# Performance work log

Hardware: AMD Instinct MI355X
Metric: run time of the kernel (lower is better)

## Reference

```python
import jax, jax.numpy as jnp
from jax import lax
import numpy as np

B, C, L, HOP = 16, 64, 16384, 256
KS = 3        # LVC / conv kernel size
DIL = 3       # static Conv1d dilation (init arg)
KL = L // HOP # kernel_length (number of conditioning frames)


def setup_inputs() -> dict:
    key = jax.random.key(0)
    k0, k1, k2, k3 = jax.random.split(key, 4)
    return {
        "hidden_states": jax.random.normal(k0, (B, C, L), jnp.float32),
        "kernel": jax.random.normal(k1, (B, C, 2 * C, KS, KL), jnp.float32) * 0.05,
        "bias": jax.random.normal(k2, (B, 2 * C, KL), jnp.float32) * 0.05,
        "conv_w": jax.random.normal(k3, (C, C, KS), jnp.float32) * 0.05,
        "conv_b": jnp.zeros((C,), jnp.float32),
        "hop_size": HOP,
    }


def _lvc(x, kernel, bias, hop_size):
    # location-variable convolution; forward() uses dilation=1 here
    b, c, length = x.shape
    _, _, out_ch, ksize, klen = kernel.shape
    pad = (ksize - 1) // 2
    xp = jnp.pad(x, ((0, 0), (0, 0), (pad, pad)))
    # sliding windows of size ksize, stride 1 -> (b, c, length, ksize)
    win = jnp.stack([xp[:, :, i:i + length] for i in range(ksize)], axis=-1)
    # split time into (kernel_length, hop_size) frames
    win = win.reshape(b, c, klen, hop_size, ksize)
    # per-frame conv kernel contraction
    o = jnp.einsum('bilsk,biokl->bols', win, kernel)  # (b, out_ch, klen, hop)
    o = o + bias[:, :, :, None]
    return o.reshape(b, out_ch, klen * hop_size)


def reference(hidden_states, kernel, bias, conv_w, conv_b, hop_size):
    slope = 0.2
    pad = DIL * (KS - 1) // 2
    residual = hidden_states
    h = jax.nn.leaky_relu(hidden_states, slope)
    h = lax.conv_general_dilated(
        h, conv_w, window_strides=(1,), padding=[(pad, pad)],
        rhs_dilation=(DIL,), dimension_numbers=('NCH', 'OIH', 'NCH'))
    h = h + conv_b[None, :, None]
    h = jax.nn.leaky_relu(h, slope)
    h = _lvc(h, kernel, bias, hop_size)
    c = residual.shape[1]
    h = jax.nn.sigmoid(h[:, :c, :]) * jnp.tanh(h[:, c:, :])  # GLU gate
    return residual + h
```

## Files before the change

### kernel.cpp

```cpp
#include <hip/hip_runtime.h>
#include <hip/hip_bf16.h>

#define TB 256

typedef __attribute__((ext_vector_type(8))) short short8;
typedef __attribute__((ext_vector_type(4))) unsigned int uint4v;
typedef __attribute__((ext_vector_type(4))) float f32x4;

#define KTF_BYTES 50331648ull
#define WS_NEED   (KTF_BYTES + 24576ull)

static __device__ __forceinline__ float lrelu(float v){ return v > 0.f ? v : 0.2f*v; }

static __device__ __forceinline__ unsigned int pack2(float lo, float hi){
    __hip_bfloat162 h = __float22bfloat162_rn(float2{lo, hi});
    unsigned int r;
    __builtin_memcpy(&r, &h, 4);
    return r;
}

static __device__ __forceinline__ float bf2f(unsigned int u16v){
    return __uint_as_float(u16v << 16);
}

static __device__ __forceinline__ float glu_gate(float a, float t){
    float u = __expf(-a);
    float v = __expf(2.0f * t);
    float den = (1.0f + u) * (v + 1.0f);
    return (v - 1.0f) * __builtin_amdgcn_rcpf(den);
}


__global__ __launch_bounds__(256, 4)
void ktf_transpose(const float* __restrict__ kern, unsigned int* __restrict__ ktf)
{
    __shared__ unsigned int tl32[128 * 65];
    const int tid = threadIdx.x;
    const int blk = blockIdx.x;
    const int k   = blk % 3;
    const int ci2 = (blk / 3) % 32;
    const int b   = blk / 96;
    const int kk  = k*2 + (ci2 >> 4);
    const int hi  = (ci2 >> 2) & 3;
    const int jp  = ci2 & 3;

    const float* src0 = kern + (size_t)b*1572864 + (size_t)ci2*49152 + k*64;
    #pragma unroll
    for (int it = 0; it < 8; ++it) {
        int p = tid + it*TB;
        int oc = p >> 4, fq = p & 15;
        const float* s = src0 + oc*192 + fq*4;
        float4 v0 = *(const float4*)(s);
        float4 v1 = *(const float4*)(s + 24576);
        unsigned int* d = tl32 + oc*65 + fq*4;
        d[0] = pack2(v0.x, v1.x);
        d[1] = pack2(v0.y, v1.y);
        d[2] = pack2(v0.z, v1.z);
        d[3] = pack2(v0.w, v1.w);
    }
    __syncthreads();

    const int l = tid & 63, wvv = tid >> 6;
    const int c = (kk*4 + jp)*4 + hi;
    const int oc0 = 2*l;
    const int slot0 = (oc0 < 64)
        ? ((oc0 >> 3)*16 + ((oc0 & 7) >> 1)*4)
        : (((oc0 - 64) >> 3)*16 + (((oc0 - 64) & 7) >> 1)*4 + 2);
    unsigned int* dst = ktf + (size_t)(b*96 + c)*8192 + slot0;
    const int f0 = wvv*16;
    #pragma unroll
    for (int fi = 0; fi < 16; ++fi) {
        int f = f0 + fi;
        uint2 v;
        v.x = tl32[(oc0    )*65 + f];
        v.y = tl32[(oc0 + 1)*65 + f];
        *(uint2*)(dst + f*128) = v;
    }
}

__global__ __launch_bounds__(256, 4)
void wf_prep(const float* __restrict__ conv_w, unsigned int* __restrict__ wf)
{
    int u = blockIdx.x*TB + threadIdx.x;
    int ln = u & 63, mt = (u >> 6) & 3, jp = (u >> 8) & 3, kk = u >> 10;
    int lo = ln & 15, hi = ln >> 4;
    int m  = mt*16 + lo;
    int k  = kk >> 1, ci = (kk & 1)*32 + hi*8 + jp*2;
    float a0 = conv_w[m*192 + ci*3 + k];
    float a1 = conv_w[m*192 + (ci + 1)*3 + k];
    wf[u] = pack2(a0, a1);
}

#define LDS_HT   18432
#define LDS_BIAS 36864

__global__ __launch_bounds__(512, 6)
void fused_kernel(const float* __restrict__ x,
                  const float* __restrict__ bias,
                  const float* __restrict__ conv_b,
                  const unsigned int* __restrict__ ktf,
                  const unsigned int* __restrict__ wf,
                  float* __restrict__ out)
{
    __shared__ char lds[37376];
    float* bias_lds = (float*)(lds + LDS_BIAS);

    const int tid = threadIdx.x;
    const int blk = blockIdx.x;
    const int h = blk & 1;
    const int bf = blk >> 1;
    const int b = bf >> 6, f = bf & 63;
    const int t0 = f << 8;
    const int tb = t0 + h*128;
    const int ln = tid & 63, wv = tid >> 6;
    const int lo = ln & 15, hi = ln >> 4;
    const int mt = wv & 3, nth = wv >> 2;

    if (tid < 128) bias_lds[tid] = bias[(size_t)b*8192 + tid*64 + f];

    {
        const float* xb = x + ((size_t)b*64 + wv*8) * 16384;
        const int ts = tb - 12;
        const bool interior = (ts >= 0) & (ts + 143 < 16384);
        #pragma unroll
        for (int it = 0; it < 3; ++it) {
            int p = (it < 2) ? (ln + it*64) : (128 + ln);
            if (it < 2 || ln < 16) {
                int t = ts + p;
                float v[8];
                if (interior) {
                    #pragma unroll
                    for (int j = 0; j < 8; ++j) v[j] = xb[j*16384 + t];
                } else {
                    bool ok = (unsigned)t < 16384u;
                    #pragma unroll
                    for (int j = 0; j < 8; ++j) v[j] = ok ? xb[j*16384 + t] : 0.f;
                }
                unsigned int w0 = pack2(lrelu(v[0]), lrelu(v[1]));
                unsigned int w1 = pack2(lrelu(v[2]), lrelu(v[3]));
                unsigned int w2 = pack2(lrelu(v[4]), lrelu(v[5]));
                unsigned int w3 = pack2(lrelu(v[6]), lrelu(v[7]));
                int a = (p*128 + wv*16) ^ ((p & 7) << 4);
                *(uint4*)(lds + a) = make_uint4(w0, w1, w2, w3);
            }
        }
    }
    __syncthreads();

    {
        uint4v aw[6];
        #pragma unroll
        for (int kk = 0; kk < 6; ++kk) {
            int w0 = kk*1024 + mt*64 + ln;
            aw[kk].x = wf[w0      ]; aw[kk].y = wf[w0 + 256];
            aw[kk].z = wf[w0 + 512]; aw[kk].w = wf[w0 + 768];
        }
        float4 cb4 = *(const float4*)(conv_b + mt*16 + hi*4);
        const int n0  = nth ? 5 : 0;
        const int cnt = nth ? 4 : 5;
        int bqa[6];
        #pragma unroll
        for (int kk = 0; kk < 6; ++kk) {
            int row = n0*16 + lo + 3*(kk >> 1) + 1;
            int cib = (kk & 1)*32 + hi*8;
            bqa[kk] = (row*128 + cib*2) ^ ((row & 7) << 4);
        }
        int hta = LDS_HT + (((n0*16 + lo)*128 + (mt*16 + hi*4)*2) ^ ((lo & 7) << 4));
        int pos = tb + n0*16 + lo - 8;
        #pragma unroll 1
        for (int i = 0; i < cnt; ++i) {
            f32x4 acc = {0.f, 0.f, 0.f, 0.f};
            __builtin_amdgcn_s_setprio(1);
            #pragma unroll
            for (int kk = 0; kk < 6; ++kk) {
                short8 bq = *(const short8*)(lds + bqa[kk]);
                acc = __builtin_amdgcn_mfma_f32_16x16x32_bf16(
                        __builtin_bit_cast(short8, aw[kk]), bq, acc, 0, 0, 0);
            }
            __builtin_amdgcn_s_setprio(0);

            bool valid = (unsigned)pos < 16384u;
            unsigned int h01 = valid ? pack2(lrelu(acc[0] + cb4.x), lrelu(acc[1] + cb4.y)) : 0u;
            unsigned int h23 = valid ? pack2(lrelu(acc[2] + cb4.z), lrelu(acc[3] + cb4.w)) : 0u;
            unsigned int* d = (unsigned int*)(lds + hta);
            d[0] = h01; d[1] = h23;

            #pragma unroll
            for (int kk = 0; kk < 6; ++kk) bqa[kk] += 2048;
            hta += 2048; pos += 16;
        }
    }
    __syncthreads();

    {
        uint4v am[6];
        const unsigned int* kp = ktf + (size_t)b*786432 + hi*8192 + f*128 + wv*16 + lo;
        #pragma unroll
        for (int kk = 0; kk < 6; ++kk) {
            int o = kk*131072;
            am[kk].x = kp[o        ]; am[kk].y = kp[o + 32768];
            am[kk].z = kp[o + 65536]; am[kk].w = kp[o + 98304];
        }
        const int c0 = wv*8;
        const int ch2 = c0 + 2*hi;
        float bs0 = bias_lds[ch2],      bs1 = bias_lds[ch2 + 1];
        float bt0 = bias_lds[ch2 + 64], bt1 = bias_lds[ch2 + 65];

        int bqa[6];
        #pragma unroll
        for (int kk = 0; kk < 6; ++kk) {
            int row = lo + 7 + (kk >> 1);
            int cib = (kk & 1)*32 + hi*8;
            bqa[kk] = LDS_HT + ((row*128 + cib*2) ^ ((row & 7) << 4));
        }
        int q  = lo + 12;
        int ra = (q*128 + ch2*2) ^ ((q & 7) << 4);
        float* ob = out + ((size_t)b*64 + ch2)*16384 + tb + lo;

        #pragma unroll 1
        for (int i = 0; i < 8; ++i) {
            f32x4 acc = {0.f, 0.f, 0.f, 0.f};
            __builtin_amdgcn_s_setprio(1);
            #pragma unroll
            for (int kk = 0; kk < 6; ++kk) {
                short8 bq = *(const short8*)(lds + bqa[kk]);
                acc = __builtin_amdgcn_mfma_f32_16x16x32_bf16(
                        __builtin_bit_cast(short8, am[kk]), bq, acc, 0, 0, 0);
            }
            __builtin_amdgcn_s_setprio(0);

            unsigned int rv = *(const unsigned int*)(lds + ra);
            float h0 = bf2f(rv & 0xFFFFu), h1 = bf2f(rv >> 16);
            float xr0 = fminf(h0, 5.0f*h0);
            float xr1 = fminf(h1, 5.0f*h1);

            float g0 = glu_gate(acc[0] + bs0, acc[2] + bt0);
            float g1 = glu_gate(acc[1] + bs1, acc[3] + bt1);
            ob[(size_t)i*16]           = xr0 + g0;
            ob[16384 + (size_t)i*16]   = xr1 + g1;

            #pragma unroll
            for (int kk = 0; kk < 6; ++kk) bqa[kk] += 2048;
            ra += 2048;
        }
    }
}

extern "C" void kernel_launch(void* const* d_in, const int* in_sizes, int n_in,
                              void* d_out, int out_size, void* d_ws, size_t ws_size,
                              hipStream_t stream)
{
    const float* x      = (const float*)d_in[0];
    const float* kern   = (const float*)d_in[1];
    const float* bias   = (const float*)d_in[2];
    const float* conv_b = (const float*)d_in[4];
    float* out = (float*)d_out;

    if (ws_size < WS_NEED) return;

    unsigned int* ktf = (unsigned int*)d_ws;
    unsigned int* wf  = (unsigned int*)((char*)d_ws + KTF_BYTES);

    wf_prep      <<<dim3(24),   dim3(TB), 0, stream>>>((const float*)d_in[3], wf);
    ktf_transpose<<<dim3(1536), dim3(TB), 0, stream>>>(kern, ktf);
    fused_kernel <<<dim3(2048), dim3(512), 0, stream>>>(x, bias, conv_b, ktf, wf, out);
    (void)in_sizes; (void)n_in; (void)out_size;
}
```

Baseline: 83.83 us.

## Give each wave two M-tiles sharing B fragments and reorder block-to-frame mapping

Each wave now computes two 16-row output tiles per LDS B-fragment read, in both the dilated conv stage and the LVC stage. This halves the LDS reads per MFMA and gives two independent accumulator chains that can interleave. Work is split across waves along the time dimension instead. The block index mapping also changes so the two half-frames of a frame are 1024 blocks apart rather than adjacent. Register use doubles for the A fragments, so the launch bound minimum occupancy drops from 6 to 4, which may reduce latency hiding.

New measurement: 90.73 us. 8.2% more time.

```diff
diff --git a/kernel.cpp b/kernel.cpp
--- a/kernel.cpp
+++ b/kernel.cpp
@@ -94,7 +94,7 @@
 #define LDS_HT   18432
 #define LDS_BIAS 36864
 
-__global__ __launch_bounds__(512, 6)
+__global__ __launch_bounds__(512, 4)
 void fused_kernel(const float* __restrict__ x,
                   const float* __restrict__ bias,
                   const float* __restrict__ conv_b,
@@ -107,14 +107,12 @@
 
     const int tid = threadIdx.x;
     const int blk = blockIdx.x;
-    const int h = blk & 1;
-    const int bf = blk >> 1;
+    const int h  = blk >> 10;
+    const int bf = blk & 1023;
     const int b = bf >> 6, f = bf & 63;
-    const int t0 = f << 8;
-    const int tb = t0 + h*128;
+    const int tb = (f << 8) + h*128;
     const int ln = tid & 63, wv = tid >> 6;
     const int lo = ln & 15, hi = ln >> 4;
-    const int mt = wv & 3, nth = wv >> 2;
 
     if (tid < 128) bias_lds[tid] = bias[(size_t)b*8192 + tid*64 + f];
 
@@ -148,16 +146,21 @@
     __syncthreads();
 
     {
-        uint4v aw[6];
-        #pragma unroll
-        for (int kk = 0; kk < 6; ++kk) {
-            int w0 = kk*1024 + mt*64 + ln;
-            aw[kk].x = wf[w0      ]; aw[kk].y = wf[w0 + 256];
-            aw[kk].z = wf[w0 + 512]; aw[kk].w = wf[w0 + 768];
-        }
-        float4 cb4 = *(const float4*)(conv_b + mt*16 + hi*4);
-        const int n0  = nth ? 5 : 0;
-        const int cnt = nth ? 4 : 5;
+        const int mp = wv & 1, nq = wv >> 1;
+        const int mtA = 2*mp, mtB = 2*mp + 1;
+        uint4v aw0[6], aw1[6];
+        #pragma unroll
+        for (int kk = 0; kk < 6; ++kk) {
+            int w0 = kk*1024 + mtA*64 + ln;
+            aw0[kk].x = wf[w0      ]; aw0[kk].y = wf[w0 + 256];
+            aw0[kk].z = wf[w0 + 512]; aw0[kk].w = wf[w0 + 768];
+            aw1[kk].x = wf[w0 +  64]; aw1[kk].y = wf[w0 + 320];
+            aw1[kk].z = wf[w0 + 576]; aw1[kk].w = wf[w0 + 832];
+        }
+        float4 cbA = *(const float4*)(conv_b + mtA*16 + hi*4);
+        float4 cbB = *(const float4*)(conv_b + mtB*16 + hi*4);
+        const int n0  = (nq == 0) ? 0 : (2*nq + 1);
+        const int cnt = (nq == 0) ? 3 : 2;
         int bqa[6];
         #pragma unroll
         for (int kk = 0; kk < 6; ++kk) {
@@ -165,83 +168,102 @@
             int cib = (kk & 1)*32 + hi*8;
             bqa[kk] = (row*128 + cib*2) ^ ((row & 7) << 4);
         }
-        int hta = LDS_HT + (((n0*16 + lo)*128 + (mt*16 + hi*4)*2) ^ ((lo & 7) << 4));
-        int pos = tb + n0*16 + lo - 8;
+        int htaA = LDS_HT + (((n0*16 + lo)*128 + (mtA*16 + hi*4)*2) ^ ((lo & 7) << 4));
+        int htaB = LDS_HT + (((n0*16 + lo)*128 + (mtB*16 + hi*4)*2) ^ ((lo & 7) << 4));
+        int pos  = tb + n0*16 + lo - 8;
         #pragma unroll 1
         for (int i = 0; i < cnt; ++i) {
-            f32x4 acc = {0.f, 0.f, 0.f, 0.f};
+            f32x4 accA = {0.f,0.f,0.f,0.f}, accB = {0.f,0.f,0.f,0.f};
             __builtin_amdgcn_s_setprio(1);
             #pragma unroll
             for (int kk = 0; kk < 6; ++kk) {
                 short8 bq = *(const short8*)(lds + bqa[kk]);
-                acc = __builtin_amdgcn_mfma_f32_16x16x32_bf16(
-                        __builtin_bit_cast(short8, aw[kk]), bq, acc, 0, 0, 0);
+                accA = __builtin_amdgcn_mfma_f32_16x16x32_bf16(
+                        __builtin_bit_cast(short8, aw0[kk]), bq, accA, 0, 0, 0);
+                accB = __builtin_amdgcn_mfma_f32_16x16x32_bf16(
+                        __builtin_bit_cast(short8, aw1[kk]), bq, accB, 0, 0, 0);
             }
             __builtin_amdgcn_s_setprio(0);
 
             bool valid = (unsigned)pos < 16384u;
-            unsigned int h01 = valid ? pack2(lrelu(acc[0] + cb4.x), lrelu(acc[1] + cb4.y)) : 0u;
-            unsigned int h23 = valid ? pack2(lrelu(acc[2] + cb4.z), lrelu(acc[3] + cb4.w)) : 0u;
-            unsigned int* d = (unsigned int*)(lds + hta);
-            d[0] = h01; d[1] = h23;
+            unsigned int* dA = (unsigned int*)(lds + htaA);
+            dA[0] = valid ? pack2(lrelu(accA[0] + cbA.x), lrelu(accA[1] + cbA.y)) : 0u;
+            dA[1] = valid ? pack2(lrelu(accA[2] + cbA.z), lrelu(accA[3] + cbA.w)) : 0u;
+            unsigned int* dB = (unsigned int*)(lds + htaB);
+            dB[0] = valid ? pack2(lrelu(accB[0] + cbB.x), lrelu(accB[1] + cbB.y)) : 0u;
+            dB[1] = valid ? pack2(lrelu(accB[2] + cbB.z), lrelu(accB[3] + cbB.w)) : 0u;
 
             #pragma unroll
             for (int kk = 0; kk < 6; ++kk) bqa[kk] += 2048;
-            hta += 2048; pos += 16;
+            htaA += 2048; htaB += 2048; pos += 16;
         }
     }
     __syncthreads();
 
     {
-        uint4v am[6];
-        const unsigned int* kp = ktf + (size_t)b*786432 + hi*8192 + f*128 + wv*16 + lo;
+        const int mtA = wv & 3, nh = wv >> 2;
+        uint4v am0[6], am1[6];
+        const unsigned int* kp = ktf + (size_t)b*786432 + hi*8192 + f*128 + mtA*16 + lo;
         #pragma unroll
         for (int kk = 0; kk < 6; ++kk) {
             int o = kk*131072;
-            am[kk].x = kp[o        ]; am[kk].y = kp[o + 32768];
-            am[kk].z = kp[o + 65536]; am[kk].w = kp[o + 98304];
-        }
-        const int c0 = wv*8;
-        const int ch2 = c0 + 2*hi;
-        float bs0 = bias_lds[ch2],      bs1 = bias_lds[ch2 + 1];
-        float bt0 = bias_lds[ch2 + 64], bt1 = bias_lds[ch2 + 65];
+            am0[kk].x = kp[o         ]; am0[kk].y = kp[o + 32768];
+            am0[kk].z = kp[o +  65536]; am0[kk].w = kp[o + 98304];
+            am1[kk].x = kp[o +     64]; am1[kk].y = kp[o + 32832];
+            am1[kk].z = kp[o +  65600]; am1[kk].w = kp[o + 98368];
+        }
+        const int ch2A = mtA*8 + 2*hi;
+        const int ch2B = ch2A + 32;
+        float bsA0 = bias_lds[ch2A],      bsA1 = bias_lds[ch2A + 1];
+        float btA0 = bias_lds[ch2A + 64], btA1 = bias_lds[ch2A + 65];
+        float bsB0 = bias_lds[ch2B],      bsB1 = bias_lds[ch2B + 1];
+        float btB0 = bias_lds[ch2B + 64], btB1 = bias_lds[ch2B + 65];
 
         int bqa[6];
         #pragma unroll
         for (int kk = 0; kk < 6; ++kk) {
-            int row = lo + 7 + (kk >> 1);
+            int row = nh*64 + lo + 7 + (kk >> 1);
             int cib = (kk & 1)*32 + hi*8;
             bqa[kk] = LDS_HT + ((row*128 + cib*2) ^ ((row & 7) << 4));
         }
-        int q  = lo + 12;
-        int ra = (q*128 + ch2*2) ^ ((q & 7) << 4);
-        float* ob = out + ((size_t)b*64 + ch2)*16384 + tb + lo;
+        int q   = nh*64 + lo + 12;
+        int raA = (q*128 + ch2A*2) ^ ((q & 7) << 4);
+        int raB = (q*128 + ch2B*2) ^ ((q & 7) << 4);
+        float* obA = out + ((size_t)b*64 + ch2A)*16384 + tb + nh*64 + lo;
+        float* obB = obA + (size_t)32*16384;
 
         #pragma unroll 1
-        for (int i = 0; i < 8; ++i) {
-            f32x4 acc = {0.f, 0.f, 0.f, 0.f};
+        for (int i = 0; i < 4; ++i) {
+            f32x4 accA = {0.f,0.f,0.f,0.f}, accB = {0.f,0.f,0.f,0.f};
             __builtin_amdgcn_s_setprio(1);
             #pragma unroll
             for (int kk = 0; kk < 6; ++kk) {
                 short8 bq = *(const short8*)(lds + bqa[kk]);
-                acc = __builtin_amdgcn_mfma_f32_16x16x32_bf16(
-                        __builtin_bit_cast(short8, am[kk]), bq, acc, 0, 0, 0);
+                accA = __builtin_amdgcn_mfma_f32_16x16x32_bf16(
+                        __builtin_bit_cast(short8, am0[kk]), bq, accA, 0, 0, 0);
+                accB = __builtin_amdgcn_mfma_f32_16x16x32_bf16(
+                        __builtin_bit_cast(short8, am1[kk]), bq, accB, 0, 0, 0);
             }
             __builtin_amdgcn_s_setprio(0);
 
-            unsigned int rv = *(const unsigned int*)(lds + ra);
-            float h0 = bf2f(rv & 0xFFFFu), h1 = bf2f(rv >> 16);
-            float xr0 = fminf(h0, 5.0f*h0);
-            float xr1 = fminf(h1, 5.0f*h1);
-
-            float g0 = glu_gate(acc[0] + bs0, acc[2] + bt0);
-            float g1 = glu_gate(acc[1] + bs1, acc[3] + bt1);
-            ob[(size_t)i*16]           = xr0 + g0;
-            ob[16384 + (size_t)i*16]   = xr1 + g1;
+            unsigned int rvA = *(const unsigned int*)(lds + raA);
+            unsigned int rvB = *(const unsigned int*)(lds + raB);
+            float hA0 = bf2f(rvA & 0xFFFFu), hA1 = bf2f(rvA >> 16);
+            float hB0 = bf2f(rvB & 0xFFFFu), hB1 = bf2f(rvB >> 16);
+
+            float gA0 = glu_gate(accA[0] + bsA0, accA[2] + btA0);
+            float gA1 = glu_gate(accA[1] + bsA1, accA[3] + btA1);
+            float gB0 = glu_gate(accB[0] + bsB0, accB[2] + btB0);
+            float gB1 = glu_gate(accB[1] + bsB1, accB[3] + btB1);
+
+            obA[(size_t)i*16]         = fminf(hA0, 5.0f*hA0) + gA0;
+            obA[16384 + (size_t)i*16] = fminf(hA1, 5.0f*hA1) + gA1;
+            obB[(size_t)i*16]         = fminf(hB0, 5.0f*hB0) + gB0;
+            obB[16384 + (size_t)i*16] = fminf(hB1, 5.0f*hB1) + gB1;
 
             #pragma unroll
             for (int kk = 0; kk < 6; ++kk) bqa[kk] += 2048;
-            ra += 2048;
+            raA += 2048; raB += 2048;
         }
     }
 }
```

## Software-pipeline LDS operand loads and hoist global weight loads ahead of barriers

Applied to the files above, without the earlier changes.

Restructures the fused kernel so that global loads for the conv weights and LVC kernel fragments are issued earlier and overlap with LDS staging and the preceding stage. Both MFMA loops are fully unrolled and double-buffer their LDS B-operand reads one iteration ahead. The occupancy hint in launch_bounds drops from 6 to 4 to make room for the extra live registers. The intent is to hide global and LDS latency, at the cost of lower occupancy and higher register pressure.

Result: slower. 86.45 us (+3.1%).

```diff
diff --git a/kernel.cpp b/kernel.cpp
--- a/kernel.cpp
+++ b/kernel.cpp
@@ -94,7 +94,7 @@
 #define LDS_HT   18432
 #define LDS_BIAS 36864
 
-__global__ __launch_bounds__(512, 6)
+__global__ __launch_bounds__(512, 4)
 void fused_kernel(const float* __restrict__ x,
                   const float* __restrict__ bias,
                   const float* __restrict__ conv_b,
@@ -110,51 +110,59 @@
     const int h = blk & 1;
     const int bf = blk >> 1;
     const int b = bf >> 6, f = bf & 63;
-    const int t0 = f << 8;
-    const int tb = t0 + h*128;
+    const int tb = (f << 8) + h*128;
     const int ln = tid & 63, wv = tid >> 6;
     const int lo = ln & 15, hi = ln >> 4;
     const int mt = wv & 3, nth = wv >> 2;
 
-    if (tid < 128) bias_lds[tid] = bias[(size_t)b*8192 + tid*64 + f];
-
-    {
-        const float* xb = x + ((size_t)b*64 + wv*8) * 16384;
-        const int ts = tb - 12;
+    const float* xb = x + ((size_t)b*64 + wv*8) * 16384;
+    const int ts = tb - 12;
+    float xv[3][8];
+    {
         const bool interior = (ts >= 0) & (ts + 143 < 16384);
         #pragma unroll
         for (int it = 0; it < 3; ++it) {
             int p = (it < 2) ? (ln + it*64) : (128 + ln);
             if (it < 2 || ln < 16) {
                 int t = ts + p;
-                float v[8];
                 if (interior) {
                     #pragma unroll
-                    for (int j = 0; j < 8; ++j) v[j] = xb[j*16384 + t];
+                    for (int j = 0; j < 8; ++j) xv[it][j] = xb[j*16384 + t];
                 } else {
                     bool ok = (unsigned)t < 16384u;
                     #pragma unroll
-                    for (int j = 0; j < 8; ++j) v[j] = ok ? xb[j*16384 + t] : 0.f;
+                    for (int j = 0; j < 8; ++j) xv[it][j] = ok ? xb[j*16384 + t] : 0.f;
                 }
-                unsigned int w0 = pack2(lrelu(v[0]), lrelu(v[1]));
-                unsigned int w1 = pack2(lrelu(v[2]), lrelu(v[3]));
-                unsigned int w2 = pack2(lrelu(v[4]), lrelu(v[5]));
-                unsigned int w3 = pack2(lrelu(v[6]), lrelu(v[7]));
-                int a = (p*128 + wv*16) ^ ((p & 7) << 4);
-                *(uint4*)(lds + a) = make_uint4(w0, w1, w2, w3);
             }
         }
     }
+    __builtin_amdgcn_sched_barrier(0);
+
+    uint4v aw[6];
+    #pragma unroll
+    for (int kk = 0; kk < 6; ++kk) {
+        int w0 = kk*1024 + mt*64 + ln;
+        aw[kk].x = wf[w0      ]; aw[kk].y = wf[w0 + 256];
+        aw[kk].z = wf[w0 + 512]; aw[kk].w = wf[w0 + 768];
+    }
+    if (tid < 128) bias_lds[tid] = bias[(size_t)b*8192 + tid*64 + f];
+    __builtin_amdgcn_sched_barrier(0);
+
+    #pragma unroll
+    for (int it = 0; it < 3; ++it) {
+        int p = (it < 2) ? (ln + it*64) : (128 + ln);
+        if (it < 2 || ln < 16) {
+            unsigned int w0 = pack2(lrelu(xv[it][0]), lrelu(xv[it][1]));
+            unsigned int w1 = pack2(lrelu(xv[it][2]), lrelu(xv[it][3]));
+            unsigned int w2 = pack2(lrelu(xv[it][4]), lrelu(xv[it][5]));
+            unsigned int w3 = pack2(lrelu(xv[it][6]), lrelu(xv[it][7]));
+            int a = (p*128 + wv*16) ^ ((p & 7) << 4);
+            *(uint4*)(lds + a) = make_uint4(w0, w1, w2, w3);
+        }
+    }
     __syncthreads();
 
     {
-        uint4v aw[6];
-        #pragma unroll
-        for (int kk = 0; kk < 6; ++kk) {
-            int w0 = kk*1024 + mt*64 + ln;
-            aw[kk].x = wf[w0      ]; aw[kk].y = wf[w0 + 256];
-            aw[kk].z = wf[w0 + 512]; aw[kk].w = wf[w0 + 768];
-        }
         float4 cb4 = *(const float4*)(conv_b + mt*16 + hi*4);
         const int n0  = nth ? 5 : 0;
         const int cnt = nth ? 4 : 5;
@@ -165,35 +173,42 @@
             int cib = (kk & 1)*32 + hi*8;
             bqa[kk] = (row*128 + cib*2) ^ ((row & 7) << 4);
         }
-        int hta = LDS_HT + (((n0*16 + lo)*128 + (mt*16 + hi*4)*2) ^ ((lo & 7) << 4));
-        int pos = tb + n0*16 + lo - 8;
-        #pragma unroll 1
-        for (int i = 0; i < cnt; ++i) {
-            f32x4 acc = {0.f, 0.f, 0.f, 0.f};
-            __builtin_amdgcn_s_setprio(1);
-            #pragma unroll
-            for (int kk = 0; kk < 6; ++kk) {
-                short8 bq = *(const short8*)(lds + bqa[kk]);
-                acc = __builtin_amdgcn_mfma_f32_16x16x32_bf16(
-                        __builtin_bit_cast(short8, aw[kk]), bq, acc, 0, 0, 0);
+        const int hta0 = LDS_HT + (((n0*16 + lo)*128 + (mt*16 + hi*4)*2) ^ ((lo & 7) << 4));
+        const int pos0 = tb + n0*16 + lo - 8;
+
+        short8 bw[2][6];
+        #pragma unroll
+        for (int kk = 0; kk < 6; ++kk)
+            bw[0][kk] = *(const short8*)(lds + bqa[kk]);
+
+        #pragma unroll
+        for (int i = 0; i < 5; ++i) {
+            if (i < cnt) {
+                if (i + 1 < cnt) {
+                    #pragma unroll
+                    for (int kk = 0; kk < 6; ++kk)
+                        bw[(i+1)&1][kk] = *(const short8*)(lds + bqa[kk] + (i+1)*2048);
+                }
+                f32x4 acc = {0.f, 0.f, 0.f, 0.f};
+                __builtin_amdgcn_s_setprio(1);
+                #pragma unroll
+                for (int kk = 0; kk < 6; ++kk)
+                    acc = __builtin_amdgcn_mfma_f32_16x16x32_bf16(
+                            __builtin_bit_cast(short8, aw[kk]), bw[i&1][kk], acc, 0, 0, 0);
+                __builtin_amdgcn_s_setprio(0);
+
+                int pos = pos0 + i*16;
+                bool valid = (unsigned)pos < 16384u;
+                unsigned int h01 = valid ? pack2(lrelu(acc[0] + cb4.x), lrelu(acc[1] + cb4.y)) : 0u;
+                unsigned int h23 = valid ? pack2(lrelu(acc[2] + cb4.z), lrelu(acc[3] + cb4.w)) : 0u;
+                unsigned int* d = (unsigned int*)(lds + hta0 + i*2048);
+                d[0] = h01; d[1] = h23;
             }
-            __builtin_amdgcn_s_setprio(0);
-
-            bool valid = (unsigned)pos < 16384u;
-            unsigned int h01 = valid ? pack2(lrelu(acc[0] + cb4.x), lrelu(acc[1] + cb4.y)) : 0u;
-            unsigned int h23 = valid ? pack2(lrelu(acc[2] + cb4.z), lrelu(acc[3] + cb4.w)) : 0u;
-            unsigned int* d = (unsigned int*)(lds + hta);
-            d[0] = h01; d[1] = h23;
-
-            #pragma unroll
-            for (int kk = 0; kk < 6; ++kk) bqa[kk] += 2048;
-            hta += 2048; pos += 16;
-        }
-    }
-    __syncthreads();
-
-    {
-        uint4v am[6];
+        }
+    }
+
+    uint4v am[6];
+    {
         const unsigned int* kp = ktf + (size_t)b*786432 + hi*8192 + f*128 + wv*16 + lo;
         #pragma unroll
         for (int kk = 0; kk < 6; ++kk) {
@@ -201,8 +216,11 @@
             am[kk].x = kp[o        ]; am[kk].y = kp[o + 32768];
             am[kk].z = kp[o + 65536]; am[kk].w = kp[o + 98304];
         }
-        const int c0 = wv*8;
-        const int ch2 = c0 + 2*hi;
+    }
+    __syncthreads();
+
+    {
+        const int ch2 = wv*8 + 2*hi;
         float bs0 = bias_lds[ch2],      bs1 = bias_lds[ch2 + 1];
         float bt0 = bias_lds[ch2 + 64], bt1 = bias_lds[ch2 + 65];
 
@@ -213,35 +231,39 @@
             int cib = (kk & 1)*32 + hi*8;
             bqa[kk] = LDS_HT + ((row*128 + cib*2) ^ ((row & 7) << 4));
         }
-        int q  = lo + 12;
-        int ra = (q*128 + ch2*2) ^ ((q & 7) << 4);
+        const int q  = lo + 12;
+        const int ra = (q*128 + ch2*2) ^ ((q & 7) << 4);
         float* ob = out + ((size_t)b*64 + ch2)*16384 + tb + lo;
 
-        #pragma unroll 1
+        short8 cq[2][6];
+        unsigned int rv[2];
+        #pragma unroll
+        for (int kk = 0; kk < 6; ++kk)
+            cq[0][kk] = *(const short8*)(lds + bqa[kk]);
+        rv[0] = *(const unsigned int*)(lds + ra);
+
+        #pragma unroll
         for (int i = 0; i < 8; ++i) {
+            unsigned int rvc = rv[i&1];
+            if (i < 7) {
+                #pragma unroll
+                for (int kk = 0; kk < 6; ++kk)
+                    cq[(i+1)&1][kk] = *(const short8*)(lds + bqa[kk] + (i+1)*2048);
+                rv[(i+1)&1] = *(const unsigned int*)(lds + ra + (i+1)*2048);
+            }
             f32x4 acc = {0.f, 0.f, 0.f, 0.f};
             __builtin_amdgcn_s_setprio(1);
             #pragma unroll
-            for (int kk = 0; kk < 6; ++kk) {
-                short8 bq = *(const short8*)(lds + bqa[kk]);
+            for (int kk = 0; kk < 6; ++kk)
                 acc = __builtin_amdgcn_mfma_f32_16x16x32_bf16(
-                        __builtin_bit_cast(short8, am[kk]), bq, acc, 0, 0, 0);
-            }
+                        __builtin_bit_cast(short8, am[kk]), cq[i&1][kk], acc, 0, 0, 0);
             __builtin_amdgcn_s_setprio(0);
 
-            unsigned int rv = *(const unsigned int*)(lds + ra);
-            float h0 = bf2f(rv & 0xFFFFu), h1 = bf2f(rv >> 16);
-            float xr0 = fminf(h0, 5.0f*h0);
-            float xr1 = fminf(h1, 5.0f*h1);
-
+            float h0 = bf2f(rvc & 0xFFFFu), h1 = bf2f(rvc >> 16);
             float g0 = glu_gate(acc[0] + bs0, acc[2] + bt0);
             float g1 = glu_gate(acc[1] + bs1, acc[3] + bt1);
-            ob[(size_t)i*16]           = xr0 + g0;
-            ob[16384 + (size_t)i*16]   = xr1 + g1;
-
-            #pragma unroll
-            for (int kk = 0; kk < 6; ++kk) bqa[kk] += 2048;
-            ra += 2048;
+            ob[(size_t)i*16]           = fminf(h0, 5.0f*h0) + g0;
+            ob[16384 + (size_t)i*16]   = fminf(h1, 5.0f*h1) + g1;
         }
     }
 }
```

## Process both half-frames per block with prefetched x tile double-buffered in LDS

Applied to the files above, without the earlier changes.

Each block now handles a whole 256-sample frame in two 128-sample halves instead of splitting halves across two blocks. The LVC kernel fragments (am) and bias are loaded once per frame and reused for both halves. The second half's x input is prefetched into registers while the first half computes, then stored into a second LDS buffer. The grid is halved, LDS grows to about 55 KB and launch bounds drop to 4 blocks per SM, which trades occupancy and parallelism for reuse and overlap.

New measurement: 96.92 us. 15.6% more time.

```diff
diff --git a/kernel.cpp b/kernel.cpp
--- a/kernel.cpp
+++ b/kernel.cpp
@@ -91,10 +91,137 @@
     wf[u] = pack2(a0, a1);
 }
 
-#define LDS_HT   18432
-#define LDS_BIAS 36864
-
-__global__ __launch_bounds__(512, 6)
+#define LDS_XT1  18432
+#define LDS_HT   36864
+#define LDS_BIAS 55296
+
+#define X_LOAD(TS_, XV_)                                                      \
+    do {                                                                      \
+        const int ts_ = (TS_);                                                \
+        const bool inter_ = (ts_ >= 0) & (ts_ + 143 < 16384);                 \
+        if (inter_) {                                                         \
+            _Pragma("unroll")                                                 \
+            for (int it = 0; it < 2; ++it)                                    \
+                if (it == 0 || ln < 8) {                                      \
+                    int t = ts_ + 2*ln + it*128;                              \
+                    _Pragma("unroll")                                         \
+                    for (int j = 0; j < 8; ++j)                               \
+                        XV_[it][j] = *(const float2*)(xb + j*16384 + t);      \
+                }                                                             \
+        } else {                                                              \
+            _Pragma("unroll")                                                 \
+            for (int it = 0; it < 2; ++it)                                    \
+                if (it == 0 || ln < 8) {                                      \
+                    int t = ts_ + 2*ln + it*128;                              \
+                    _Pragma("unroll")                                         \
+                    for (int j = 0; j < 8; ++j) {                             \
+                        float a0_ = ((unsigned)t       < 16384u) ? xb[j*16384 + t    ] : 0.f; \
+                        float a1_ = ((unsigned)(t + 1) < 16384u) ? xb[j*16384 + t + 1] : 0.f; \
+                        XV_[it][j] = make_float2(a0_, a1_);                   \
+                    }                                                         \
+                }                                                             \
+        }                                                                     \
+    } while (0)
+
+#define X_STORE(XTB_, XV_)                                                    \
+    do {                                                                      \
+        _Pragma("unroll")                                                     \
+        for (int it = 0; it < 2; ++it)                                        \
+            if (it == 0 || ln < 8) {                                          \
+                int p0 = 2*ln + it*128;                                       \
+                unsigned int w0_[4], w1_[4];                                  \
+                _Pragma("unroll")                                             \
+                for (int jq = 0; jq < 4; ++jq) {                              \
+                    float2 e0_ = XV_[it][2*jq], e1_ = XV_[it][2*jq + 1];      \
+                    w0_[jq] = pack2(lrelu(e0_.x), lrelu(e1_.x));              \
+                    w1_[jq] = pack2(lrelu(e0_.y), lrelu(e1_.y));              \
+                }                                                             \
+                int a0_ = (XTB_) + (( p0     *128 + wv*16) ^ (( p0      & 7) << 4)); \
+                int a1_ = (XTB_) + (((p0 + 1)*128 + wv*16) ^ (((p0 + 1) & 7) << 4)); \
+                *(uint4*)(lds + a0_) = make_uint4(w0_[0], w0_[1], w0_[2], w0_[3]); \
+                *(uint4*)(lds + a1_) = make_uint4(w1_[0], w1_[1], w1_[2], w1_[3]); \
+            }                                                                 \
+    } while (0)
+
+#define B_PHASE(XTB_, TB_)                                                    \
+    do {                                                                      \
+        uint4v aw_[6];                                                        \
+        _Pragma("unroll")                                                     \
+        for (int kk = 0; kk < 6; ++kk) {                                      \
+            int w0_ = kk*1024 + mt*64 + ln;                                   \
+            aw_[kk].x = wf[w0_      ]; aw_[kk].y = wf[w0_ + 256];             \
+            aw_[kk].z = wf[w0_ + 512]; aw_[kk].w = wf[w0_ + 768];             \
+        }                                                                     \
+        float4 cb4_ = *(const float4*)(conv_b + mt*16 + hi*4);                \
+        const int n0_  = nth ? 5 : 0;                                         \
+        const int cnt_ = nth ? 4 : 5;                                         \
+        int bqa_[6];                                                          \
+        _Pragma("unroll")                                                     \
+        for (int kk = 0; kk < 6; ++kk) {                                      \
+            int row_ = n0_*16 + lo + 3*(kk >> 1) + 1;                         \
+            int cib_ = (kk & 1)*32 + hi*8;                                    \
+            bqa_[kk] = (XTB_) + ((row_*128 + cib_*2) ^ ((row_ & 7) << 4));    \
+        }                                                                     \
+        int hta_ = LDS_HT + (((n0_*16 + lo)*128 + (mt*16 + hi*4)*2) ^ ((lo & 7) << 4)); \
+        int pos_ = (TB_) + n0_*16 + lo - 8;                                   \
+        _Pragma("unroll 1")                                                   \
+        for (int i = 0; i < cnt_; ++i) {                                      \
+            f32x4 acc_ = {0.f, 0.f, 0.f, 0.f};                                \
+            __builtin_amdgcn_s_setprio(1);                                    \
+            _Pragma("unroll")                                                 \
+            for (int kk = 0; kk < 6; ++kk) {                                  \
+                short8 bq_ = *(const short8*)(lds + bqa_[kk]);                \
+                acc_ = __builtin_amdgcn_mfma_f32_16x16x32_bf16(               \
+                        __builtin_bit_cast(short8, aw_[kk]), bq_, acc_, 0, 0, 0); \
+            }                                                                 \
+            __builtin_amdgcn_s_setprio(0);                                    \
+            bool valid_ = (unsigned)pos_ < 16384u;                            \
+            unsigned int h01_ = valid_ ? pack2(lrelu(acc_[0] + cb4_.x), lrelu(acc_[1] + cb4_.y)) : 0u; \
+            unsigned int h23_ = valid_ ? pack2(lrelu(acc_[2] + cb4_.z), lrelu(acc_[3] + cb4_.w)) : 0u; \
+            unsigned int* d_ = (unsigned int*)(lds + hta_);                   \
+            d_[0] = h01_; d_[1] = h23_;                                       \
+            _Pragma("unroll")                                                 \
+            for (int kk = 0; kk < 6; ++kk) bqa_[kk] += 2048;                  \
+            hta_ += 2048; pos_ += 16;                                         \
+        }                                                                     \
+    } while (0)
+
+#define C_PHASE(XTB_, TB_)                                                    \
+    do {                                                                      \
+        int bqa_[6];                                                          \
+        _Pragma("unroll")                                                     \
+        for (int kk = 0; kk < 6; ++kk) {                                      \
+            int row_ = lo + 7 + (kk >> 1);                                    \
+            int cib_ = (kk & 1)*32 + hi*8;                                    \
+            bqa_[kk] = LDS_HT + ((row_*128 + cib_*2) ^ ((row_ & 7) << 4));    \
+        }                                                                     \
+        const int q_  = lo + 12;                                              \
+        int ra_ = (XTB_) + ((q_*128 + ch2*2) ^ ((q_ & 7) << 4));              \
+        float* ob_ = out + ((size_t)b*64 + ch2)*16384 + (TB_) + lo;           \
+        _Pragma("unroll 1")                                                   \
+        for (int i = 0; i < 8; ++i) {                                         \
+            f32x4 acc_ = {0.f, 0.f, 0.f, 0.f};                                \
+            __builtin_amdgcn_s_setprio(1);                                    \
+            _Pragma("unroll")                                                 \
+            for (int kk = 0; kk < 6; ++kk) {                                  \
+                short8 bq_ = *(const short8*)(lds + bqa_[kk]);                \
+                acc_ = __builtin_amdgcn_mfma_f32_16x16x32_bf16(               \
+                        __builtin_bit_cast(short8, am[kk]), bq_, acc_, 0, 0, 0); \
+            }                                                                 \
+            __builtin_amdgcn_s_setprio(0);                                    \
+            unsigned int rvc_ = *(const unsigned int*)(lds + ra_);            \
+            float h0_ = bf2f(rvc_ & 0xFFFFu), h1_ = bf2f(rvc_ >> 16);         \
+            float g0_ = glu_gate(acc_[0] + bs0, acc_[2] + bt0);               \
+            float g1_ = glu_gate(acc_[1] + bs1, acc_[3] + bt1);               \
+            ob_[(size_t)i*16]         = fminf(h0_, 5.0f*h0_) + g0_;           \
+            ob_[16384 + (size_t)i*16] = fminf(h1_, 5.0f*h1_) + g1_;           \
+            _Pragma("unroll")                                                 \
+            for (int kk = 0; kk < 6; ++kk) bqa_[kk] += 2048;                  \
+            ra_ += 2048;                                                      \
+        }                                                                     \
+    } while (0)
+
+__global__ __launch_bounds__(512, 4)
 void fused_kernel(const float* __restrict__ x,
                   const float* __restrict__ bias,
                   const float* __restrict__ conv_b,
@@ -102,98 +229,25 @@
                   const unsigned int* __restrict__ wf,
                   float* __restrict__ out)
 {
-    __shared__ char lds[37376];
+    __shared__ char lds[55808];
     float* bias_lds = (float*)(lds + LDS_BIAS);
 
     const int tid = threadIdx.x;
     const int blk = blockIdx.x;
-    const int h = blk & 1;
-    const int bf = blk >> 1;
-    const int b = bf >> 6, f = bf & 63;
+    const int b = blk >> 6, f = blk & 63;
     const int t0 = f << 8;
-    const int tb = t0 + h*128;
     const int ln = tid & 63, wv = tid >> 6;
     const int lo = ln & 15, hi = ln >> 4;
     const int mt = wv & 3, nth = wv >> 2;
 
-    if (tid < 128) bias_lds[tid] = bias[(size_t)b*8192 + tid*64 + f];
-
+    const float* xb = x + ((size_t)b*64 + wv*8) * 16384;
+    float2 xv[2][8];
+
+    X_LOAD(t0 - 12, xv);
+    __builtin_amdgcn_sched_barrier(0);
+
+    uint4v am[6];
     {
-        const float* xb = x + ((size_t)b*64 + wv*8) * 16384;
-        const int ts = tb - 12;
-        const bool interior = (ts >= 0) & (ts + 143 < 16384);
-        #pragma unroll
-        for (int it = 0; it < 3; ++it) {
-            int p = (it < 2) ? (ln + it*64) : (128 + ln);
-            if (it < 2 || ln < 16) {
-                int t = ts + p;
-                float v[8];
-                if (interior) {
-                    #pragma unroll
-                    for (int j = 0; j < 8; ++j) v[j] = xb[j*16384 + t];
-                } else {
-                    bool ok = (unsigned)t < 16384u;
-                    #pragma unroll
-                    for (int j = 0; j < 8; ++j) v[j] = ok ? xb[j*16384 + t] : 0.f;
-                }
-                unsigned int w0 = pack2(lrelu(v[0]), lrelu(v[1]));
-                unsigned int w1 = pack2(lrelu(v[2]), lrelu(v[3]));
-                unsigned int w2 = pack2(lrelu(v[4]), lrelu(v[5]));
-                unsigned int w3 = pack2(lrelu(v[6]), lrelu(v[7]));
-                int a = (p*128 + wv*16) ^ ((p & 7) << 4);
-                *(uint4*)(lds + a) = make_uint4(w0, w1, w2, w3);
-            }
-        }
-    }
-    __syncthreads();
-
-    {
-        uint4v aw[6];
-        #pragma unroll
-        for (int kk = 0; kk < 6; ++kk) {
-            int w0 = kk*1024 + mt*64 + ln;
-            aw[kk].x = wf[w0      ]; aw[kk].y = wf[w0 + 256];
-            aw[kk].z = wf[w0 + 512]; aw[kk].w = wf[w0 + 768];
-        }
-        float4 cb4 = *(const float4*)(conv_b + mt*16 + hi*4);
-        const int n0  = nth ? 5 : 0;
-        const int cnt = nth ? 4 : 5;
-        int bqa[6];
-        #pragma unroll
-        for (int kk = 0; kk < 6; ++kk) {
-            int row = n0*16 + lo + 3*(kk >> 1) + 1;
-            int cib = (kk & 1)*32 + hi*8;
-            bqa[kk] = (row*128 + cib*2) ^ ((row & 7) << 4);
-        }
-        int hta = LDS_HT + (((n0*16 + lo)*128 + (mt*16 + hi*4)*2) ^ ((lo & 7) << 4));
-        int pos = tb + n0*16 + lo - 8;
-        #pragma unroll 1
-        for (int i = 0; i < cnt; ++i) {
-            f32x4 acc = {0.f, 0.f, 0.f, 0.f};
-            __builtin_amdgcn_s_setprio(1);
-            #pragma unroll
-            for (int kk = 0; kk < 6; ++kk) {
-                short8 bq = *(const short8*)(lds + bqa[kk]);
-                acc = __builtin_amdgcn_mfma_f32_16x16x32_bf16(
-                        __builtin_bit_cast(short8, aw[kk]), bq, acc, 0, 0, 0);
-            }
-            __builtin_amdgcn_s_setprio(0);
-
-            bool valid = (unsigned)pos < 16384u;
-            unsigned int h01 = valid ? pack2(lrelu(acc[0] + cb4.x), lrelu(acc[1] + cb4.y)) : 0u;
-            unsigned int h23 = valid ? pack2(lrelu(acc[2] + cb4.z), lrelu(acc[3] + cb4.w)) : 0u;
-            unsigned int* d = (unsigned int*)(lds + hta);
-            d[0] = h01; d[1] = h23;
-
-            #pragma unroll
-            for (int kk = 0; kk < 6; ++kk) bqa[kk] += 2048;
-            hta += 2048; pos += 16;
-        }
-    }
-    __syncthreads();
-
-    {
-        uint4v am[6];
         const unsigned int* kp = ktf + (size_t)b*786432 + hi*8192 + f*128 + wv*16 + lo;
         #pragma unroll
         for (int kk = 0; kk < 6; ++kk) {
@@ -201,49 +255,29 @@
             am[kk].x = kp[o        ]; am[kk].y = kp[o + 32768];
             am[kk].z = kp[o + 65536]; am[kk].w = kp[o + 98304];
         }
-        const int c0 = wv*8;
-        const int ch2 = c0 + 2*hi;
-        float bs0 = bias_lds[ch2],      bs1 = bias_lds[ch2 + 1];
-        float bt0 = bias_lds[ch2 + 64], bt1 = bias_lds[ch2 + 65];
-
-        int bqa[6];
-        #pragma unroll
-        for (int kk = 0; kk < 6; ++kk) {
-            int row = lo + 7 + (kk >> 1);
-            int cib = (kk & 1)*32 + hi*8;
-            bqa[kk] = LDS_HT + ((row*128 + cib*2) ^ ((row & 7) << 4));
-        }
-        int q  = lo + 12;
-        int ra = (q*128 + ch2*2) ^ ((q & 7) << 4);
-        float* ob = out + ((size_t)b*64 + ch2)*16384 + tb + lo;
-
-        #pragma unroll 1
-        for (int i = 0; i < 8; ++i) {
-            f32x4 acc = {0.f, 0.f, 0.f, 0.f};
-            __builtin_amdgcn_s_setprio(1);
-            #pragma unroll
-            for (int kk = 0; kk < 6; ++kk) {
-                short8 bq = *(const short8*)(lds + bqa[kk]);
-                acc = __builtin_amdgcn_mfma_f32_16x16x32_bf16(
-                        __builtin_bit_cast(short8, am[kk]), bq, acc, 0, 0, 0);
-            }
-            __builtin_amdgcn_s_setprio(0);
-
-            unsigned int rv = *(const unsigned int*)(lds + ra);
-            float h0 = bf2f(rv & 0xFFFFu), h1 = bf2f(rv >> 16);
-            float xr0 = fminf(h0, 5.0f*h0);
-            float xr1 = fminf(h1, 5.0f*h1);
-
-            float g0 = glu_gate(acc[0] + bs0, acc[2] + bt0);
-            float g1 = glu_gate(acc[1] + bs1, acc[3] + bt1);
-            ob[(size_t)i*16]           = xr0 + g0;
-            ob[16384 + (size_t)i*16]   = xr1 + g1;
-
-            #pragma unroll
-            for (int kk = 0; kk < 6; ++kk) bqa[kk] += 2048;
-            ra += 2048;
-        }
     }
+    if (tid < 128) bias_lds[tid] = bias[(size_t)b*8192 + tid*64 + f];
+    __builtin_amdgcn_sched_barrier(0);
+
+    X_STORE(0, xv);
+    __syncthreads();
+
+    const int ch2 = wv*8 + 2*hi;
+    const float bs0 = bias_lds[ch2],      bs1 = bias_lds[ch2 + 1];
+    const float bt0 = bias_lds[ch2 + 64], bt1 = bias_lds[ch2 + 65];
+
+    X_LOAD(t0 + 116, xv);
+    __builtin_amdgcn_sched_barrier(0);
+
+    B_PHASE(0, t0);
+    __syncthreads();
+    C_PHASE(0, t0);
+    X_STORE(LDS_XT1, xv);
+    __syncthreads();
+
+    B_PHASE(LDS_XT1, t0 + 128);
+    __syncthreads();
+    C_PHASE(LDS_XT1, t0 + 128);
 }
 
 extern "C" void kernel_launch(void* const* d_in, const int* in_sizes, int n_in,
@@ -263,6 +297,6 @@
 
     wf_prep      <<<dim3(24),   dim3(TB), 0, stream>>>((const float*)d_in[3], wf);
     ktf_transpose<<<dim3(1536), dim3(TB), 0, stream>>>(kern, ktf);
-    fused_kernel <<<dim3(2048), dim3(512), 0, stream>>>(x, bias, conv_b, ktf, wf, out);
+    fused_kernel <<<dim3(1024), dim3(512), 0, stream>>>(x, bias, conv_b, ktf, wf, out);
     (void)in_sizes; (void)n_in; (void)out_size;
 }
```
